# Optimization experiments

Measured on AMD Instinct MI355X. Metric: run time of the kernel, lower is better.

## Reference

```python
import jax, jax.numpy as jnp
import numpy as np

N = 262144          # total points
IN_DIM = 9
OUT_DIM = 256
FDIM = 128
MAX_PT = 64
B, GX, GY, GZ = 4, 64, 64, 16
EPS = 1e-5


def _linear_params(key, fin, fout):
    k1, k2 = jax.random.split(key)
    bound = 1.0 / np.sqrt(fin)
    w = jax.random.uniform(k1, (fin, fout), minval=-bound, maxval=bound, dtype=jnp.float32)
    b = jax.random.uniform(k2, (fout,), minval=-bound, maxval=bound, dtype=jnp.float32)
    return w, b


def setup_inputs() -> dict:
    key = jax.random.key(0)
    ks = jax.random.split(key, 12)
    pt_fea = jax.random.normal(ks[0], (N, IN_DIM), dtype=jnp.float32)
    bidx = jax.random.randint(ks[1], (N, 1), 0, B, dtype=jnp.int32)
    gx = jax.random.randint(ks[2], (N, 1), 0, GX, dtype=jnp.int32)
    gy = jax.random.randint(ks[3], (N, 1), 0, GY, dtype=jnp.int32)
    gz = jax.random.randint(ks[4], (N, 1), 0, GZ, dtype=jnp.int32)
    pt_ind = jnp.concatenate([bidx, gx, gy, gz], axis=1)
    # emulate torch.randperm shuffle (fixed seed)
    perm = jax.random.permutation(ks[5], N)
    pt_fea = pt_fea[perm]
    pt_ind = pt_ind[perm]
    w1, b1 = _linear_params(ks[6], IN_DIM, 64)
    w2, b2 = _linear_params(ks[7], 64, 128)
    w3, b3 = _linear_params(ks[8], 128, 256)
    w4, b4 = _linear_params(ks[9], 256, OUT_DIM)
    wc, bc = _linear_params(ks[10], OUT_DIM, FDIM)
    return {
        'pt_fea': pt_fea, 'pt_ind': pt_ind,
        'bn0_g': jnp.ones(IN_DIM), 'bn0_b': jnp.zeros(IN_DIM),
        'w1': w1, 'b1': b1, 'bn1_g': jnp.ones(64), 'bn1_b': jnp.zeros(64),
        'w2': w2, 'b2': b2, 'bn2_g': jnp.ones(128), 'bn2_b': jnp.zeros(128),
        'w3': w3, 'b3': b3, 'bn3_g': jnp.ones(256), 'bn3_b': jnp.zeros(256),
        'w4': w4, 'b4': b4, 'wc': wc, 'bc': bc,
    }


def _masked_bn(x, g, b, mf):
    # BatchNorm1d in training mode, statistics over kept points only (biased var)
    w = mf[:, None]
    n = jnp.sum(mf)
    mean = jnp.sum(x * w, axis=0) / n
    var = jnp.sum(jnp.square(x - mean) * w, axis=0) / n
    return (x - mean) * jax.lax.rsqrt(var + EPS) * g + b


def _grouping(pt_ind):
    # encode (batch, x, y, z) rows into a single int key; lexicographic order preserved
    keys = ((pt_ind[:, 0] * GX + pt_ind[:, 1]) * GY + pt_ind[:, 2]) * GZ + pt_ind[:, 3]
    unq, unq_inv = jnp.unique(keys, return_inverse=True, size=N, fill_value=-1)
    cnt = jax.ops.segment_sum(jnp.ones(N, jnp.int32), unq_inv, num_segments=N)
    valid = cnt > 0
    # rank of each point within its voxel group (stable order -> matches grp_range_torch)
    order = jnp.argsort(unq_inv, stable=True)
    sorted_inv = unq_inv[order]
    firstpos = jax.ops.segment_min(jnp.arange(N, dtype=jnp.int32), sorted_inv,
                                   num_segments=N, indices_are_sorted=True)
    grp_sorted = jnp.arange(N, dtype=jnp.int32) - firstpos[sorted_inv]
    grp = jnp.zeros(N, jnp.int32).at[order].set(grp_sorted)
    mask = grp < MAX_PT
    # decode unique keys back to coordinates [N, 4] (padded rows -> -1)
    z = unq % GZ; t = unq // GZ
    y = t % GY; t = t // GY
    x = t % GX; bb = t // GX
    coords = jnp.stack([bb, x, y, z], axis=1).astype(jnp.int64)
    coords = jnp.where(valid[:, None], coords, -1)
    return unq_inv, valid, mask, coords


def reference(pt_fea, pt_ind, bn0_g, bn0_b, w1, b1, bn1_g, bn1_b, w2, b2,
              bn2_g, bn2_b, w3, b3, bn3_g, bn3_b, w4, b4, wc, bc):
    unq_inv, valid, mask, coords = _grouping(pt_ind)
    mf = mask.astype(pt_fea.dtype)
    h = _masked_bn(pt_fea, bn0_g, bn0_b, mf)
    h = jax.nn.relu(_masked_bn(h @ w1 + b1, bn1_g, bn1_b, mf))
    h = jax.nn.relu(_masked_bn(h @ w2 + b2, bn2_g, bn2_b, mf))
    h = jax.nn.relu(_masked_bn(h @ w3 + b3, bn3_g, bn3_b, mf))
    h = h @ w4 + b4                                   # [N, OUT_DIM]
    feat = jnp.where(mask[:, None], h, -jnp.inf)      # drop points beyond MAX_PT per voxel
    pooled = jax.ops.segment_max(feat, unq_inv, num_segments=N)
    pooled = jnp.where(valid[:, None], pooled, 0.0)   # zero padded voxel slots
    voxel_features = jax.nn.relu(pooled @ wc + bc)    # [N, FDIM], rows beyond n_unique padded
    return coords, voxel_features
```

## Files before the change

### kernel.cpp

```cpp
#include <hip/hip_runtime.h>
#include <hip/hip_bf16.h>
#include <math.h>

#define N_PTS 262144
#define SBLOCKS 1024

typedef short short8 __attribute__((ext_vector_type(8)));
typedef float f32x4 __attribute__((ext_vector_type(4)));

__device__ __forceinline__ unsigned short f2bf(float f) {
    unsigned u = __float_as_uint(f);
    u = u + 0x7fff + ((u >> 16) & 1);
    return (unsigned short)(u >> 16);
}

__global__ void k_keys(const int* __restrict__ pt_ind, int* __restrict__ key, int* __restrict__ cnt) {
    int i = blockIdx.x * 256 + threadIdx.x;
    int b = pt_ind[i * 4 + 0], x = pt_ind[i * 4 + 1], y = pt_ind[i * 4 + 2], z = pt_ind[i * 4 + 3];
    int k = ((b * 64 + x) * 64 + y) * 16 + z;
    key[i] = k;
    atomicAdd(&cnt[k], 1);
}

__global__ __launch_bounds__(1024) void k_scan1(const int* __restrict__ cnt, int* __restrict__ rank,
                                                int* __restrict__ startb, int2* __restrict__ bsums) {
    __shared__ int so[1024], sc[1024];
    int t = threadIdx.x;
    int g = blockIdx.x * 1024 + t;
    int c = cnt[g];
    int o = (c > 0) ? 1 : 0;
    so[t] = o; sc[t] = c;
    __syncthreads();
    for (int off = 1; off < 1024; off <<= 1) {
        int vo = (t >= off) ? so[t - off] : 0;
        int vc = (t >= off) ? sc[t - off] : 0;
        __syncthreads();
        if (t >= off) { so[t] += vo; sc[t] += vc; }
        __syncthreads();
    }
    rank[g] = so[t] - o;
    startb[g] = sc[t] - c;
    if (t == 1023) bsums[blockIdx.x] = make_int2(so[t], sc[t]);
}

__global__ void k_scan2(int2* __restrict__ bsums, int* __restrict__ devU) {
    __shared__ int so[256], sc[256];
    int t = threadIdx.x;
    int2 v = bsums[t];
    so[t] = v.x; sc[t] = v.y;
    __syncthreads();
    for (int off = 1; off < 256; off <<= 1) {
        int vo = (t >= off) ? so[t - off] : 0;
        int vc = (t >= off) ? sc[t - off] : 0;
        __syncthreads();
        if (t >= off) { so[t] += vo; sc[t] += vc; }
        __syncthreads();
    }
    bsums[t] = make_int2(so[t] - v.x, sc[t] - v.y);
    if (t == 255) *devU = so[255];
}

__global__ __launch_bounds__(1024) void k_scan3(int* __restrict__ rank, int* __restrict__ startb,
                                                const int2* __restrict__ bsums) {
    int g = blockIdx.x * 1024 + threadIdx.x;
    int2 o = bsums[blockIdx.x];
    rank[g] += o.x;
    startb[g] += o.y;
}

__global__ void k_scatter(const int* __restrict__ key, const int* __restrict__ startb,
                          int* __restrict__ cursor, int* __restrict__ bucket) {
    int i = blockIdx.x * 256 + threadIdx.x;
    int k = key[i];
    int pos = startb[k] + atomicAdd(&cursor[k], 1);
    bucket[pos] = i;
}

__global__ void k_grouprank(const int* __restrict__ bucket, const int* __restrict__ key,
                            const int* __restrict__ cnt, const int* __restrict__ startb,
                            int* __restrict__ maskb_s, int* __restrict__ maskb_o,
                            int* __restrict__ n_masked) {
    int pos = blockIdx.x * 256 + threadIdx.x;
    int i = bucket[pos];
    int k = key[i];
    int s = startb[k];
    int c = cnt[k];
    int g = 0;
    for (int j = 0; j < c; j++) {
        int p = bucket[s + j];
        g += (p < i) ? 1 : 0;
    }
    int m = (g < 64) ? 1 : 0;
    maskb_s[pos] = m;
    maskb_o[i] = m;
    unsigned long long bal = __ballot(m);
    if ((threadIdx.x & 63) == 0) atomicAdd(n_masked, (int)__popcll(bal));
}

__global__ void k_coords(const int* __restrict__ cnt, const int* __restrict__ rank,
                         const int* __restrict__ startb, const int* __restrict__ devU,
                         float* __restrict__ out, int* __restrict__ ustart, int* __restrict__ ucnt) {
    int k = blockIdx.x * 256 + threadIdx.x;
    int U = *devU;
    if (cnt[k] > 0) {
        int r = rank[k];
        int z = k & 15;
        int t = k >> 4;
        int y = t & 63; t >>= 6;
        int x = t & 63;
        int b = t >> 6;
        out[r * 4 + 0] = (float)b;
        out[r * 4 + 1] = (float)x;
        out[r * 4 + 2] = (float)y;
        out[r * 4 + 3] = (float)z;
        ustart[r] = startb[k];
        ucnt[r] = cnt[k];
    }
    if (k >= U) {
        out[k * 4 + 0] = -1.f;
        out[k * 4 + 1] = -1.f;
        out[k * 4 + 2] = -1.f;
        out[k * 4 + 3] = -1.f;
    }
}

template<int F, int FP>
__global__ __launch_bounds__(256) void k_stats(const float* __restrict__ buf, const int* __restrict__ maskb,
                                               float* __restrict__ psum, float* __restrict__ psq) {
    constexpr int RG = 256 / FP;
    int tid = threadIdx.x;
    int col = tid % FP;
    int rg = tid / FP;
    constexpr int RPB = N_PTS / SBLOCKS;
    int r0 = blockIdx.x * RPB;
    float s = 0.f, q = 0.f;
    for (int r = r0 + rg; r < r0 + RPB; r += RG) {
        float mf = (float)maskb[r];
        if (col < F) {
            float v = buf[(size_t)r * F + col];
            s += v * mf;
            q += v * v * mf;
        }
    }
    __shared__ float ls[256], lq[256];
    ls[tid] = s; lq[tid] = q;
    __syncthreads();
    for (int half = RG / 2; half > 0; half >>= 1) {
        if (rg < half) { ls[tid] += ls[tid + half * FP]; lq[tid] += lq[tid + half * FP]; }
        __syncthreads();
    }
    if (rg == 0 && col < F) {
        psum[blockIdx.x * F + col] = ls[tid];
        psq[blockIdx.x * F + col] = lq[tid];
    }
}

template<int F, int NB>
__global__ __launch_bounds__(256) void k_finalize(const float* __restrict__ psum, const float* __restrict__ psq,
                                                  const int* __restrict__ n_masked, const float* __restrict__ g,
                                                  const float* __restrict__ b, float* __restrict__ ss) {
    int j = blockIdx.x;
    int t = threadIdx.x;
    double s = 0.0, q = 0.0;
    for (int i = t; i < NB; i += 256) {
        s += (double)psum[(size_t)i * F + j];
        q += (double)psq[(size_t)i * F + j];
    }
    __shared__ double ds[256], dq[256];
    ds[t] = s; dq[t] = q;
    __syncthreads();
    for (int half = 128; half > 0; half >>= 1) {
        if (t < half) { ds[t] += ds[t + half]; dq[t] += dq[t + half]; }
        __syncthreads();
    }
    if (t == 0) {
        double n = (double)(*n_masked);
        double mean = ds[0] / n;
        double var = dq[0] / n - mean * mean;
        if (var < 0.0) var = 0.0;
        double scale = (double)g[j] / sqrt(var + 1e-5);
        ss[j * 2] = (float)scale;
        ss[j * 2 + 1] = (float)((double)b[j] - mean * scale);
    }
}

template<int K, int F>
__global__ void k_wprep(const float* __restrict__ W, const float* __restrict__ ss,
                        unsigned short* __restrict__ WH, unsigned short* __restrict__ WL,
                        float* __restrict__ c0a, float* __restrict__ c1a) {
    int idx = blockIdx.x * 256 + threadIdx.x;
    if (idx >= K * F) return;
    int k = idx / F, f = idx % F;
    float s = 1.f, t = 0.f;
    if (ss) { s = ss[k * 2]; t = ss[k * 2 + 1]; }
    float sg = (s >= 0.f) ? 1.f : -1.f;
    float as = fabsf(s);
    float c1, c0;
    if (as < 1e-30f) { c1 = 0.f; c0 = fmaxf(t, 0.f); as = 1.f; }
    else { c1 = sg; c0 = t / as; }
    if (f == 0) { c0a[k] = c0; c1a[k] = c1; }
    float wv = as * W[(size_t)k * F + f];
    unsigned u = __float_as_uint(wv);
    unsigned hk = u & 0xFFFF0000u;
    float lo = wv - __uint_as_float(hk);
    WH[(size_t)f * K + k] = (unsigned short)(hk >> 16);
    WL[(size_t)f * K + k] = f2bf(lo);
}

__global__ __launch_bounds__(256) void k_mm1(const float* __restrict__ Af, const int* __restrict__ bucket,
                                             const float* __restrict__ W, const float* __restrict__ bias,
                                             const float* __restrict__ ss, const int* __restrict__ maskb_s,
                                             float* __restrict__ out,
                                             float* __restrict__ psum, float* __restrict__ psq) {
    constexpr int K = 9, F = 64, TM = 4, TN = 4;
    constexpr int SLOTS = F / TN;
    constexpr int RG = 256 / SLOTS;
    constexpr int MT = TM * RG;
    constexpr int STRIDE = 12;
    __shared__ float As[MT * STRIDE];
    __shared__ float msk[64];
    __shared__ float rs[4][256], rq[4][256];

    int tid = threadIdx.x;
    int row0 = blockIdx.x * MT;

    if (tid < 64) msk[tid] = (float)maskb_s[row0 + tid];
    for (int idx = tid; idx < MT * K; idx += 256) {
        int r = idx / K;
        int kk = idx % K;
        int src = bucket[row0 + r];
        float v = Af[(size_t)src * K + kk];
        v = v * ss[kk * 2] + ss[kk * 2 + 1];
        As[r * STRIDE + kk] = v;
    }
    __syncthreads();

    int slot = tid % SLOTS;
    int rg = tid / SLOTS;

    float acc[TM][TN];
    #pragma unroll
    for (int m = 0; m < TM; m++)
        #pragma unroll
        for (int i = 0; i < TN; i++) acc[m][i] = 0.f;

    #pragma unroll 3
    for (int k = 0; k < K; k++) {
        float w[TN];
        #pragma unroll
        for (int i = 0; i < TN; i++) w[i] = W[k * F + slot + i * SLOTS];
        #pragma unroll
        for (int m = 0; m < TM; m++) {
            float a = As[(rg * TM + m) * STRIDE + k];
            #pragma unroll
            for (int i = 0; i < TN; i++) acc[m][i] = fmaf(a, w[i], acc[m][i]);
        }
    }

    float s4[4] = {0.f, 0.f, 0.f, 0.f}, q4[4] = {0.f, 0.f, 0.f, 0.f};
    #pragma unroll
    for (int m = 0; m < TM; m++) {
        int r = row0 + rg * TM + m;
        float mf = msk[rg * TM + m];
        #pragma unroll
        for (int i = 0; i < TN; i++) {
            int c = slot + i * SLOTS;
            float v = acc[m][i] + bias[c];
            out[(size_t)r * F + c] = v;
            float t = mf * v;
            s4[i] += t;
            q4[i] += t * v;
        }
    }
    #pragma unroll
    for (int i = 0; i < 4; i++) { rs[i][tid] = s4[i]; rq[i][tid] = q4[i]; }
    __syncthreads();
    for (int half = 8; half > 0; half >>= 1) {
        if (rg < half) {
            #pragma unroll
            for (int i = 0; i < 4; i++) {
                rs[i][tid] += rs[i][tid + half * 16];
                rq[i][tid] += rq[i][tid + half * 16];
            }
        }
        __syncthreads();
    }
    if (rg == 0) {
        #pragma unroll
        for (int i = 0; i < 4; i++) {
            psum[(size_t)blockIdx.x * F + slot + i * 16] = rs[i][tid];
            psq[(size_t)blockIdx.x * F + slot + i * 16] = rq[i][tid];
        }
    }
}

template<int K, int F, int MODE, bool AMAX, bool TBL, bool STATS>
__global__ __launch_bounds__(2 * F) void k_gemm(const float* __restrict__ A,
                                                const unsigned short* __restrict__ WH,
                                                const unsigned short* __restrict__ WL,
                                                const float* __restrict__ c0a, const float* __restrict__ c1a,
                                                const float* __restrict__ bias, const int* __restrict__ devU,
                                                const int* __restrict__ maskb, float* __restrict__ out,
                                                float* __restrict__ psum, float* __restrict__ psq) {
    constexpr int THREADS = 2 * F;
    constexpr int RPASS = THREADS / 4;
    constexpr int NPASS = 128 / RPASS;
    __shared__ unsigned AsH[128 * 32], AsL[128 * 32];
    __shared__ float msk[128];
    __shared__ float sps[F], spq[F];
    const int tid = threadIdx.x;
    const int row0 = blockIdx.x * 128;
    const int w = tid >> 6, lane = tid & 63;
    const int wm = w & 1, wn = w >> 1;
    const int lr = lane & 15, lg = lane >> 4;
    const int r0 = tid >> 2, q0 = tid & 3;

    int U = 0x7fffffff;
    if constexpr (MODE == 2) {
        U = *devU;
        if (row0 >= U) {
            for (int idx = tid; idx < 128 * F; idx += THREADS) {
                int rr = idx / F, cc = idx % F;
                out[(size_t)(row0 + rr) * F + cc] = fmaxf(bias[cc], 0.f);
            }
            return;
        }
    }

    if constexpr (STATS) { if (tid < 128) msk[tid] = (float)maskb[row0 + tid]; }

    f32x4 acc[4][4];
    #pragma unroll
    for (int m = 0; m < 4; m++)
        #pragma unroll
        for (int n = 0; n < 4; n++) acc[m][n] = (f32x4)(0.f);

    float4 ld[NPASS][4];
    #pragma unroll
    for (int un = 0; un < NPASS; ++un) {
        const float4* p4 = (const float4*)(A + (size_t)(row0 + r0 + un * RPASS) * K + q0 * 16);
        #pragma unroll
        for (int p = 0; p < 4; ++p) ld[un][p] = p4[p];
    }

    for (int kc = 0; kc < K; kc += 64) {
        float4 tc0[4], tc1[4];
        if constexpr (TBL) {
            #pragma unroll
            for (int p = 0; p < 4; ++p) {
                tc0[p] = *(const float4*)&c0a[kc + q0 * 16 + p * 4];
                tc1[p] = *(const float4*)&c1a[kc + q0 * 16 + p * 4];
            }
        }
        __syncthreads();
        #pragma unroll
        for (int un = 0; un < NPASS; ++un) {
            int r = r0 + un * RPASS;
            unsigned swz = (unsigned)((r & 7) << 2);
            bool valid = true;
            if constexpr (MODE == 2) valid = (row0 + r) < U;
            unsigned uh[8], ul[8];
            #pragma unroll
            for (int p = 0; p < 4; ++p) {
                float zz[4] = {ld[un][p].x, ld[un][p].y, ld[un][p].z, ld[un][p].w};
                #pragma unroll
                for (int e = 0; e < 4; ++e) {
                    float z = zz[e];
                    if constexpr (MODE == 2) z = valid ? z : 0.f;
                    if constexpr (TBL) z = fmaf(z, (&tc1[p].x)[e], (&tc0[p].x)[e]);
                    if constexpr (AMAX) z = fmaxf(z, 0.f);
                    zz[e] = z;
                }
                #pragma unroll
                for (int h = 0; h < 2; ++h) {
                    unsigned u0 = __float_as_uint(zz[h * 2]), u1 = __float_as_uint(zz[h * 2 + 1]);
                    unsigned hi = (u1 & 0xFFFF0000u) | (u0 >> 16);
                    float l0 = zz[h * 2]     - __uint_as_float(u0 & 0xFFFF0000u);
                    float l1 = zz[h * 2 + 1] - __uint_as_float(u1 & 0xFFFF0000u);
                    unsigned lo = ((unsigned)f2bf(l1) << 16) | (unsigned)f2bf(l0);
                    uh[p * 2 + h] = hi;
                    ul[p * 2 + h] = lo;
                }
            }
            unsigned b0 = r * 32 + ((q0 * 8 + 0) ^ swz);
            unsigned b1 = r * 32 + ((q0 * 8 + 4) ^ swz);
            *(uint4*)&AsH[b0] = make_uint4(uh[0], uh[1], uh[2], uh[3]);
            *(uint4*)&AsH[b1] = make_uint4(uh[4], uh[5], uh[6], uh[7]);
            *(uint4*)&AsL[b0] = make_uint4(ul[0], ul[1], ul[2], ul[3]);
            *(uint4*)&AsL[b1] = make_uint4(ul[4], ul[5], ul[6], ul[7]);
        }
        __syncthreads();
        if (kc + 64 < K) {
            #pragma unroll
            for (int un = 0; un < NPASS; ++un) {
                const float4* p4 = (const float4*)(A + (size_t)(row0 + r0 + un * RPASS) * K + kc + 64 + q0 * 16);
                #pragma unroll
                for (int p = 0; p < 4; ++p) ld[un][p] = p4[p];
            }
        }
        #pragma unroll
        for (int kb = 0; kb < 2; ++kb) {
            short8 bh[4], bl[4];
            #pragma unroll
            for (int n = 0; n < 4; n++) {
                int c = wn * 64 + n * 16 + lr;
                size_t off = (size_t)c * K + kc + kb * 32 + lg * 8;
                bh[n] = *(const short8*)(WH + off);
                bl[n] = *(const short8*)(WL + off);
            }
            #pragma unroll
            for (int m = 0; m < 4; m++) {
                int rr = wm * 64 + m * 16 + lr;
                unsigned base = rr * 32 + ((kb * 16 + lg * 4) ^ ((unsigned)(rr & 7) << 2));
                short8 ah = *(const short8*)&AsH[base];
                short8 al = *(const short8*)&AsL[base];
                #pragma unroll
                for (int n = 0; n < 4; n++) {
                    acc[m][n] = __builtin_amdgcn_mfma_f32_16x16x32_bf16(ah, bh[n], acc[m][n], 0, 0, 0);
                    acc[m][n] = __builtin_amdgcn_mfma_f32_16x16x32_bf16(ah, bl[n], acc[m][n], 0, 0, 0);
                    acc[m][n] = __builtin_amdgcn_mfma_f32_16x16x32_bf16(al, bh[n], acc[m][n], 0, 0, 0);
                }
            }
        }
    }

    float bn[4];
    #pragma unroll
    for (int n = 0; n < 4; n++) bn[n] = bias[wn * 64 + n * 16 + lr];

    float s4[4] = {0.f, 0.f, 0.f, 0.f}, q4[4] = {0.f, 0.f, 0.f, 0.f};
    #pragma unroll
    for (int m = 0; m < 4; m++) {
        float mf[4];
        if constexpr (STATS) {
            #pragma unroll
            for (int reg = 0; reg < 4; reg++) mf[reg] = msk[wm * 64 + m * 16 + lg * 4 + reg];
        }
        #pragma unroll
        for (int n = 0; n < 4; n++) {
            int col = wn * 64 + n * 16 + lr;
            #pragma unroll
            for (int reg = 0; reg < 4; reg++) {
                int row = row0 + wm * 64 + m * 16 + lg * 4 + reg;
                float v = acc[m][n][reg] + bn[n];
                if constexpr (MODE == 2) v = fmaxf(v, 0.f);
                out[(size_t)row * F + col] = v;
                if constexpr (STATS) { float t = mf[reg] * v; s4[n] += t; q4[n] += t * v; }
            }
        }
    }

    if constexpr (STATS) {
        #pragma unroll
        for (int n = 0; n < 4; n++) {
            s4[n] += __shfl_xor(s4[n], 16); s4[n] += __shfl_xor(s4[n], 32);
            q4[n] += __shfl_xor(q4[n], 16); q4[n] += __shfl_xor(q4[n], 32);
        }
        if (wm == 0 && lg == 0) {
            #pragma unroll
            for (int n = 0; n < 4; n++) {
                int col = wn * 64 + n * 16 + lr;
                sps[col] = s4[n]; spq[col] = q4[n];
            }
        }
        __syncthreads();
        if (wm == 1 && lg == 0) {
            #pragma unroll
            for (int n = 0; n < 4; n++) {
                int col = wn * 64 + n * 16 + lr;
                psum[(size_t)blockIdx.x * F + col] = sps[col] + s4[n];
                psq[(size_t)blockIdx.x * F + col] = spq[col] + q4[n];
            }
        }
    }
}

__global__ __launch_bounds__(256) void k_pool(const float* __restrict__ h4,
                                              const int* __restrict__ ustart, const int* __restrict__ ucnt,
                                              const int* __restrict__ maskb_s, const int* __restrict__ devU,
                                              float* __restrict__ pooled) {
    int u = blockIdx.x * 4 + (threadIdx.x >> 6);
    if (u >= *devU) return;
    int lane = threadIdx.x & 63;
    int s = ustart[u], c = ucnt[u];
    float4 v = make_float4(-3.4e38f, -3.4e38f, -3.4e38f, -3.4e38f);
    for (int j = 0; j < c; ++j) {
        int row = s + j;
        if (maskb_s[row]) {
            float4 x = *(const float4*)&h4[(size_t)row * 256 + lane * 4];
            v.x = fmaxf(v.x, x.x);
            v.y = fmaxf(v.y, x.y);
            v.z = fmaxf(v.z, x.z);
            v.w = fmaxf(v.w, x.w);
        }
    }
    *(float4*)&pooled[(size_t)u * 256 + lane * 4] = v;
}

extern "C" void kernel_launch(void* const* d_in, const int* in_sizes, int n_in,
                              void* d_out, int out_size, void* d_ws, size_t ws_size,
                              hipStream_t stream) {
    const float* pt_fea = (const float*)d_in[0];
    const int*   pt_ind = (const int*)d_in[1];
    const float* bn0_g = (const float*)d_in[2];
    const float* bn0_b = (const float*)d_in[3];
    const float* w1 = (const float*)d_in[4];
    const float* b1 = (const float*)d_in[5];
    const float* bn1_g = (const float*)d_in[6];
    const float* bn1_b = (const float*)d_in[7];
    const float* w2 = (const float*)d_in[8];
    const float* b2 = (const float*)d_in[9];
    const float* bn2_g = (const float*)d_in[10];
    const float* bn2_b = (const float*)d_in[11];
    const float* w3 = (const float*)d_in[12];
    const float* b3 = (const float*)d_in[13];
    const float* bn3_g = (const float*)d_in[14];
    const float* bn3_b = (const float*)d_in[15];
    const float* w4 = (const float*)d_in[16];
    const float* b4 = (const float*)d_in[17];
    const float* wc = (const float*)d_in[18];
    const float* bc = (const float*)d_in[19];

    float* outF = (float*)d_out;
    float* coords_out = outF;
    float* feat_out = outF + (size_t)4 * N_PTS;

    char* wp = (char*)d_ws;
    auto alloc = [&](size_t bytes) {
        char* p = wp;
        wp += (bytes + 255) & ~(size_t)255;
        return p;
    };
    float* bufA = (float*)alloc((size_t)N_PTS * 256 * 4);
    float* bufB = (float*)alloc((size_t)N_PTS * 256 * 4);
    int* key     = (int*)alloc((size_t)N_PTS * 4);
    int* cnt     = (int*)alloc((size_t)N_PTS * 4);
    int* rank    = (int*)alloc((size_t)N_PTS * 4);
    int* startb  = (int*)alloc((size_t)N_PTS * 4);
    int* cursor  = (int*)alloc((size_t)N_PTS * 4);
    int* bucket  = (int*)alloc((size_t)N_PTS * 4);
    int* maskb_s = (int*)alloc((size_t)N_PTS * 4);
    int* maskb_o = (int*)alloc((size_t)N_PTS * 4);
    int* ustart  = (int*)alloc((size_t)N_PTS * 4);
    int* ucnt    = (int*)alloc((size_t)N_PTS * 4);
    int2* bsums  = (int2*)alloc(256 * sizeof(int2));
    int* devU    = (int*)alloc(256);
    int* n_masked= (int*)alloc(256);
    float* psum  = (float*)alloc((size_t)2048 * 256 * 4);
    float* psq   = (float*)alloc((size_t)2048 * 256 * 4);
    float* ss0   = (float*)alloc(2048);
    float* ss1   = (float*)alloc(2048);
    float* ss2   = (float*)alloc(2048);
    float* ss3   = (float*)alloc(2048);
    unsigned short* W2H = (unsigned short*)alloc(64 * 128 * 2);
    unsigned short* W2L = (unsigned short*)alloc(64 * 128 * 2);
    unsigned short* W3H = (unsigned short*)alloc(128 * 256 * 2);
    unsigned short* W3L = (unsigned short*)alloc(128 * 256 * 2);
    unsigned short* W4H = (unsigned short*)alloc(256 * 256 * 2);
    unsigned short* W4L = (unsigned short*)alloc(256 * 256 * 2);
    unsigned short* WCH = (unsigned short*)alloc(256 * 128 * 2);
    unsigned short* WCL = (unsigned short*)alloc(256 * 128 * 2);
    float* c02 = (float*)alloc(64 * 4);   float* c12 = (float*)alloc(64 * 4);
    float* c03 = (float*)alloc(128 * 4);  float* c13 = (float*)alloc(128 * 4);
    float* c04 = (float*)alloc(256 * 4);  float* c14 = (float*)alloc(256 * 4);
    float* c0c = (float*)alloc(256 * 4);  float* c1c = (float*)alloc(256 * 4);

    hipMemsetAsync(cnt, 0, (size_t)N_PTS * 4, stream);
    hipMemsetAsync(cursor, 0, (size_t)N_PTS * 4, stream);
    hipMemsetAsync(n_masked, 0, 4, stream);

    k_wprep<256, 128><<<(256 * 128 + 255) / 256, 256, 0, stream>>>(wc, nullptr, WCH, WCL, c0c, c1c);

    k_keys<<<N_PTS / 256, 256, 0, stream>>>(pt_ind, key, cnt);
    k_scan1<<<N_PTS / 1024, 1024, 0, stream>>>(cnt, rank, startb, bsums);
    k_scan2<<<1, 256, 0, stream>>>(bsums, devU);
    k_scan3<<<N_PTS / 1024, 1024, 0, stream>>>(rank, startb, bsums);
    k_scatter<<<N_PTS / 256, 256, 0, stream>>>(key, startb, cursor, bucket);
    k_grouprank<<<N_PTS / 256, 256, 0, stream>>>(bucket, key, cnt, startb, maskb_s, maskb_o, n_masked);
    k_coords<<<N_PTS / 256, 256, 0, stream>>>(cnt, rank, startb, devU, coords_out, ustart, ucnt);

    k_stats<9, 16><<<SBLOCKS, 256, 0, stream>>>(pt_fea, maskb_o, psum, psq);
    k_finalize<9, SBLOCKS><<<9, 256, 0, stream>>>(psum, psq, n_masked, bn0_g, bn0_b, ss0);

    k_mm1<<<N_PTS / 64, 256, 0, stream>>>(pt_fea, bucket, w1, b1, ss0, maskb_s, bufA, psum, psq);
    k_finalize<64, N_PTS / 64><<<64, 256, 0, stream>>>(psum, psq, n_masked, bn1_g, bn1_b, ss1);
    k_wprep<64, 128><<<(64 * 128 + 255) / 256, 256, 0, stream>>>(w2, ss1, W2H, W2L, c02, c12);

    k_gemm<64, 128, 0, true, true, true><<<N_PTS / 128, 256, 0, stream>>>(
        bufA, W2H, W2L, c02, c12, b2, nullptr, maskb_s, bufB, psum, psq);
    k_finalize<128, N_PTS / 128><<<128, 256, 0, stream>>>(psum, psq, n_masked, bn2_g, bn2_b, ss2);
    k_wprep<128, 256><<<(128 * 256 + 255) / 256, 256, 0, stream>>>(w3, ss2, W3H, W3L, c03, c13);

    k_gemm<128, 256, 0, true, true, true><<<N_PTS / 128, 512, 0, stream>>>(
        bufB, W3H, W3L, c03, c13, b3, nullptr, maskb_s, bufA, psum, psq);
    k_finalize<256, N_PTS / 128><<<256, 256, 0, stream>>>(psum, psq, n_masked, bn3_g, bn3_b, ss3);
    k_wprep<256, 256><<<(256 * 256 + 255) / 256, 256, 0, stream>>>(w4, ss3, W4H, W4L, c04, c14);

    k_gemm<256, 256, 0, true, true, false><<<N_PTS / 128, 512, 0, stream>>>(
        bufA, W4H, W4L, c04, c14, b4, nullptr, nullptr, bufB, nullptr, nullptr);

    k_pool<<<N_PTS / 4, 256, 0, stream>>>(bufB, ustart, ucnt, maskb_s, devU, bufA);

    k_gemm<256, 128, 2, false, false, false><<<N_PTS / 128, 256, 0, stream>>>(
        bufA, WCH, WCL, nullptr, nullptr, bc, devU, nullptr, feat_out, nullptr, nullptr);
}
```

Before: 925.9 us.

## Double-buffer A tiles and software-pipeline B fragment loads in split-bf16 GEMM

Restructures the GEMM kernel to always use 512 threads, with each wave covering F/4 columns. A tiles are double-buffered in shared memory, and the next tile is staged partway through the current MFMA batch. B fragments are prefetched one batch ahead in two register sets, and MFMA sections raise wave priority with s_setprio. The aim is to hide global and LDS latency behind matrix math and cut barrier stalls, at the cost of double the shared memory and higher register pressure from the 4-wave occupancy hint.

```diff
diff --git a/kernel.cpp b/kernel.cpp
--- a/kernel.cpp
+++ b/kernel.cpp
@@ -295,19 +295,21 @@
 }
 
 template<int K, int F, int MODE, bool AMAX, bool TBL, bool STATS>
-__global__ __launch_bounds__(2 * F) void k_gemm(const float* __restrict__ A,
-                                                const unsigned short* __restrict__ WH,
-                                                const unsigned short* __restrict__ WL,
-                                                const float* __restrict__ c0a, const float* __restrict__ c1a,
-                                                const float* __restrict__ bias, const int* __restrict__ devU,
-                                                const int* __restrict__ maskb, float* __restrict__ out,
-                                                float* __restrict__ psum, float* __restrict__ psq) {
-    constexpr int THREADS = 2 * F;
-    constexpr int RPASS = THREADS / 4;
-    constexpr int NPASS = 128 / RPASS;
-    __shared__ unsigned AsH[128 * 32], AsL[128 * 32];
-    __shared__ float msk[128];
-    __shared__ float sps[F], spq[F];
+__global__ __launch_bounds__(512, 4) void k_gemm(const float* __restrict__ A,
+                                                 const unsigned short* __restrict__ WH,
+                                                 const unsigned short* __restrict__ WL,
+                                                 const float* __restrict__ c0a, const float* __restrict__ c1a,
+                                                 const float* __restrict__ bias, const int* __restrict__ devU,
+                                                 const int* __restrict__ maskb, float* __restrict__ out,
+                                                 float* __restrict__ psum, float* __restrict__ psq) {
+    constexpr int NN = F / 64;
+    constexpr int NB2 = NN / 2;
+    constexpr int NBATCH = 2 * NB2;
+    constexpr int NKC = K / 64;
+    constexpr int FQ = F / 4;
+    __shared__ unsigned AsH[2 * 4096], AsL[2 * 4096];
+    __shared__ float msk[STATS ? 128 : 1];
+    __shared__ float sps[STATS ? F : 1], spq[STATS ? F : 1];
     const int tid = threadIdx.x;
     const int row0 = blockIdx.x * 128;
     const int w = tid >> 6, lane = tid & 63;
@@ -319,116 +321,123 @@
     if constexpr (MODE == 2) {
         U = *devU;
         if (row0 >= U) {
-            for (int idx = tid; idx < 128 * F; idx += THREADS) {
+            for (int idx = tid; idx < 128 * F; idx += 512) {
                 int rr = idx / F, cc = idx % F;
                 out[(size_t)(row0 + rr) * F + cc] = fmaxf(bias[cc], 0.f);
             }
             return;
         }
     }
-
     if constexpr (STATS) { if (tid < 128) msk[tid] = (float)maskb[row0 + tid]; }
 
-    f32x4 acc[4][4];
+    f32x4 acc[4][NN];
     #pragma unroll
     for (int m = 0; m < 4; m++)
         #pragma unroll
-        for (int n = 0; n < 4; n++) acc[m][n] = (f32x4)(0.f);
-
-    float4 ld[NPASS][4];
-    #pragma unroll
-    for (int un = 0; un < NPASS; ++un) {
-        const float4* p4 = (const float4*)(A + (size_t)(row0 + r0 + un * RPASS) * K + q0 * 16);
-        #pragma unroll
-        for (int p = 0; p < 4; ++p) ld[un][p] = p4[p];
-    }
-
-    for (int kc = 0; kc < K; kc += 64) {
-        float4 tc0[4], tc1[4];
-        if constexpr (TBL) {
-            #pragma unroll
-            for (int p = 0; p < 4; ++p) {
-                tc0[p] = *(const float4*)&c0a[kc + q0 * 16 + p * 4];
-                tc1[p] = *(const float4*)&c1a[kc + q0 * 16 + p * 4];
-            }
-        }
-        __syncthreads();
-        #pragma unroll
-        for (int un = 0; un < NPASS; ++un) {
-            int r = r0 + un * RPASS;
-            unsigned swz = (unsigned)((r & 7) << 2);
-            bool valid = true;
-            if constexpr (MODE == 2) valid = (row0 + r) < U;
-            unsigned uh[8], ul[8];
-            #pragma unroll
-            for (int p = 0; p < 4; ++p) {
-                float zz[4] = {ld[un][p].x, ld[un][p].y, ld[un][p].z, ld[un][p].w};
-                #pragma unroll
-                for (int e = 0; e < 4; ++e) {
-                    float z = zz[e];
-                    if constexpr (MODE == 2) z = valid ? z : 0.f;
-                    if constexpr (TBL) z = fmaf(z, (&tc1[p].x)[e], (&tc0[p].x)[e]);
-                    if constexpr (AMAX) z = fmaxf(z, 0.f);
-                    zz[e] = z;
-                }
-                #pragma unroll
-                for (int h = 0; h < 2; ++h) {
-                    unsigned u0 = __float_as_uint(zz[h * 2]), u1 = __float_as_uint(zz[h * 2 + 1]);
-                    unsigned hi = (u1 & 0xFFFF0000u) | (u0 >> 16);
-                    float l0 = zz[h * 2]     - __uint_as_float(u0 & 0xFFFF0000u);
-                    float l1 = zz[h * 2 + 1] - __uint_as_float(u1 & 0xFFFF0000u);
-                    unsigned lo = ((unsigned)f2bf(l1) << 16) | (unsigned)f2bf(l0);
-                    uh[p * 2 + h] = hi;
-                    ul[p * 2 + h] = lo;
-                }
-            }
-            unsigned b0 = r * 32 + ((q0 * 8 + 0) ^ swz);
-            unsigned b1 = r * 32 + ((q0 * 8 + 4) ^ swz);
-            *(uint4*)&AsH[b0] = make_uint4(uh[0], uh[1], uh[2], uh[3]);
-            *(uint4*)&AsH[b1] = make_uint4(uh[4], uh[5], uh[6], uh[7]);
-            *(uint4*)&AsL[b0] = make_uint4(ul[0], ul[1], ul[2], ul[3]);
-            *(uint4*)&AsL[b1] = make_uint4(ul[4], ul[5], ul[6], ul[7]);
-        }
-        __syncthreads();
-        if (kc + 64 < K) {
-            #pragma unroll
-            for (int un = 0; un < NPASS; ++un) {
-                const float4* p4 = (const float4*)(A + (size_t)(row0 + r0 + un * RPASS) * K + kc + 64 + q0 * 16);
-                #pragma unroll
-                for (int p = 0; p < 4; ++p) ld[un][p] = p4[p];
-            }
-        }
-        #pragma unroll
-        for (int kb = 0; kb < 2; ++kb) {
-            short8 bh[4], bl[4];
-            #pragma unroll
-            for (int n = 0; n < 4; n++) {
-                int c = wn * 64 + n * 16 + lr;
-                size_t off = (size_t)c * K + kc + kb * 32 + lg * 8;
-                bh[n] = *(const short8*)(WH + off);
-                bl[n] = *(const short8*)(WL + off);
-            }
+        for (int n = 0; n < NN; n++) acc[m][n] = (f32x4)(0.f);
+
+    float4 ld[4];
+    auto loadA = [&](int t) {
+        const float4* p4 = (const float4*)(A + (size_t)(row0 + r0) * K + t * 64 + q0 * 16);
+        #pragma unroll
+        for (int p = 0; p < 4; ++p) ld[p] = p4[p];
+    };
+    auto stageA = [&](int buf, int t) {
+        unsigned swz = (unsigned)((r0 & 7) << 2);
+        bool valid = true;
+        if constexpr (MODE == 2) valid = (row0 + r0) < U;
+        unsigned uh[8], ul[8];
+        #pragma unroll
+        for (int p = 0; p < 4; ++p) {
+            float4 tc0, tc1;
+            if constexpr (TBL) {
+                tc0 = *(const float4*)&c0a[t * 64 + q0 * 16 + p * 4];
+                tc1 = *(const float4*)&c1a[t * 64 + q0 * 16 + p * 4];
+            }
+            float zz[4] = {ld[p].x, ld[p].y, ld[p].z, ld[p].w};
+            #pragma unroll
+            for (int e = 0; e < 4; ++e) {
+                float z = zz[e];
+                if constexpr (MODE == 2) z = valid ? z : 0.f;
+                if constexpr (TBL) z = fmaf(z, (&tc1.x)[e], (&tc0.x)[e]);
+                if constexpr (AMAX) z = fmaxf(z, 0.f);
+                zz[e] = z;
+            }
+            #pragma unroll
+            for (int h = 0; h < 2; ++h) {
+                unsigned u0 = __float_as_uint(zz[h * 2]), u1 = __float_as_uint(zz[h * 2 + 1]);
+                unsigned hi = (u1 & 0xFFFF0000u) | (u0 >> 16);
+                float l0 = zz[h * 2]     - __uint_as_float(u0 & 0xFFFF0000u);
+                float l1 = zz[h * 2 + 1] - __uint_as_float(u1 & 0xFFFF0000u);
+                unsigned lo = ((unsigned)f2bf(l1) << 16) | (unsigned)f2bf(l0);
+                uh[p * 2 + h] = hi;
+                ul[p * 2 + h] = lo;
+            }
+        }
+        unsigned b0 = buf * 4096 + r0 * 32 + ((q0 * 8 + 0) ^ swz);
+        unsigned b1 = buf * 4096 + r0 * 32 + ((q0 * 8 + 4) ^ swz);
+        *(uint4*)&AsH[b0] = make_uint4(uh[0], uh[1], uh[2], uh[3]);
+        *(uint4*)&AsH[b1] = make_uint4(uh[4], uh[5], uh[6], uh[7]);
+        *(uint4*)&AsL[b0] = make_uint4(ul[0], ul[1], ul[2], ul[3]);
+        *(uint4*)&AsL[b1] = make_uint4(ul[4], ul[5], ul[6], ul[7]);
+    };
+
+    short8 bh[2][2], bl[2][2];
+    auto loadB = [&](int t, int b, int set) {
+        int kb = b / NB2, p = b % NB2;
+        #pragma unroll
+        for (int j = 0; j < 2; ++j) {
+            int col = wn * FQ + (p * 2 + j) * 16 + lr;
+            size_t off = (size_t)col * K + t * 64 + kb * 32 + lg * 8;
+            bh[set][j] = *(const short8*)(WH + off);
+            bl[set][j] = *(const short8*)(WL + off);
+        }
+    };
+
+    loadA(0);
+    loadB(0, 0, 0);
+    stageA(0, 0);
+    if (NKC > 1) loadA(1);
+
+    for (int t = 0; t < NKC; ++t) {
+        int cur = t & 1;
+        __syncthreads();
+        #pragma unroll
+        for (int b = 0; b < NBATCH; ++b) {
+            const int kb = b / NB2, p = b % NB2;
+            const int s = b & 1;
+            if (b + 1 < NBATCH) loadB(t, b + 1, s ^ 1);
+            else if (t + 1 < NKC) loadB(t + 1, 0, s ^ 1);
+            if (b == NB2 && t + 1 < NKC) {
+                stageA(cur ^ 1, t + 1);
+                if (t + 2 < NKC) loadA(t + 2);
+            }
+            __builtin_amdgcn_s_setprio(1);
             #pragma unroll
             for (int m = 0; m < 4; m++) {
                 int rr = wm * 64 + m * 16 + lr;
-                unsigned base = rr * 32 + ((kb * 16 + lg * 4) ^ ((unsigned)(rr & 7) << 2));
+                unsigned base = cur * 4096 + rr * 32 + ((kb * 16 + lg * 4) ^ ((unsigned)(rr & 7) << 2));
                 short8 ah = *(const short8*)&AsH[base];
                 short8 al = *(const short8*)&AsL[base];
                 #pragma unroll
-                for (int n = 0; n < 4; n++) {
-                    acc[m][n] = __builtin_amdgcn_mfma_f32_16x16x32_bf16(ah, bh[n], acc[m][n], 0, 0, 0);
-                    acc[m][n] = __builtin_amdgcn_mfma_f32_16x16x32_bf16(ah, bl[n], acc[m][n], 0, 0, 0);
-                    acc[m][n] = __builtin_amdgcn_mfma_f32_16x16x32_bf16(al, bh[n], acc[m][n], 0, 0, 0);
+                for (int j = 0; j < 2; j++) {
+                    int n = p * 2 + j;
+                    acc[m][n] = __builtin_amdgcn_mfma_f32_16x16x32_bf16(ah, bh[s][j], acc[m][n], 0, 0, 0);
+                    acc[m][n] = __builtin_amdgcn_mfma_f32_16x16x32_bf16(ah, bl[s][j], acc[m][n], 0, 0, 0);
+                    acc[m][n] = __builtin_amdgcn_mfma_f32_16x16x32_bf16(al, bh[s][j], acc[m][n], 0, 0, 0);
                 }
             }
-        }
-    }
-
-    float bn[4];
+            __builtin_amdgcn_s_setprio(0);
+        }
+    }
+
+    float bn[NN];
     #pragma unroll
-    for (int n = 0; n < 4; n++) bn[n] = bias[wn * 64 + n * 16 + lr];
-
-    float s4[4] = {0.f, 0.f, 0.f, 0.f}, q4[4] = {0.f, 0.f, 0.f, 0.f};
+    for (int n = 0; n < NN; n++) bn[n] = bias[wn * FQ + n * 16 + lr];
+
+    float s4[NN], q4[NN];
+    #pragma unroll
+    for (int n = 0; n < NN; n++) { s4[n] = 0.f; q4[n] = 0.f; }
     #pragma unroll
     for (int m = 0; m < 4; m++) {
         float mf[4];
@@ -437,37 +446,37 @@
             for (int reg = 0; reg < 4; reg++) mf[reg] = msk[wm * 64 + m * 16 + lg * 4 + reg];
         }
         #pragma unroll
-        for (int n = 0; n < 4; n++) {
-            int col = wn * 64 + n * 16 + lr;
+        for (int n = 0; n < NN; n++) {
+            int col = wn * FQ + n * 16 + lr;
             #pragma unroll
             for (int reg = 0; reg < 4; reg++) {
                 int row = row0 + wm * 64 + m * 16 + lg * 4 + reg;
                 float v = acc[m][n][reg] + bn[n];
                 if constexpr (MODE == 2) v = fmaxf(v, 0.f);
                 out[(size_t)row * F + col] = v;
-                if constexpr (STATS) { float t = mf[reg] * v; s4[n] += t; q4[n] += t * v; }
+                if constexpr (STATS) { float tt = mf[reg] * v; s4[n] += tt; q4[n] += tt * v; }
             }
         }
     }
 
     if constexpr (STATS) {
         #pragma unroll
-        for (int n = 0; n < 4; n++) {
+        for (int n = 0; n < NN; n++) {
             s4[n] += __shfl_xor(s4[n], 16); s4[n] += __shfl_xor(s4[n], 32);
             q4[n] += __shfl_xor(q4[n], 16); q4[n] += __shfl_xor(q4[n], 32);
         }
         if (wm == 0 && lg == 0) {
             #pragma unroll
-            for (int n = 0; n < 4; n++) {
-                int col = wn * 64 + n * 16 + lr;
+            for (int n = 0; n < NN; n++) {
+                int col = wn * FQ + n * 16 + lr;
                 sps[col] = s4[n]; spq[col] = q4[n];
             }
         }
         __syncthreads();
         if (wm == 1 && lg == 0) {
             #pragma unroll
-            for (int n = 0; n < 4; n++) {
-                int col = wn * 64 + n * 16 + lr;
+            for (int n = 0; n < NN; n++) {
+                int col = wn * FQ + n * 16 + lr;
                 psum[(size_t)blockIdx.x * F + col] = sps[col] + s4[n];
                 psq[(size_t)blockIdx.x * F + col] = spq[col] + q4[n];
             }
@@ -586,7 +595,7 @@
     k_finalize<64, N_PTS / 64><<<64, 256, 0, stream>>>(psum, psq, n_masked, bn1_g, bn1_b, ss1);
     k_wprep<64, 128><<<(64 * 128 + 255) / 256, 256, 0, stream>>>(w2, ss1, W2H, W2L, c02, c12);
 
-    k_gemm<64, 128, 0, true, true, true><<<N_PTS / 128, 256, 0, stream>>>(
+    k_gemm<64, 128, 0, true, true, true><<<N_PTS / 128, 512, 0, stream>>>(
         bufA, W2H, W2L, c02, c12, b2, nullptr, maskb_s, bufB, psum, psq);
     k_finalize<128, N_PTS / 128><<<128, 256, 0, stream>>>(psum, psq, n_masked, bn2_g, bn2_b, ss2);
     k_wprep<128, 256><<<(128 * 256 + 255) / 256, 256, 0, stream>>>(w3, ss2, W3H, W3L, c03, c13);
@@ -601,6 +610,6 @@
 
     k_pool<<<N_PTS / 4, 256, 0, stream>>>(bufB, ustart, ucnt, maskb_s, devU, bufA);
 
-    k_gemm<256, 128, 2, false, false, false><<<N_PTS / 128, 256, 0, stream>>>(
+    k_gemm<256, 128, 2, false, false, false><<<N_PTS / 128, 512, 0, stream>>>(
         bufA, WCH, WCL, nullptr, nullptr, bc, devU, nullptr, feat_out, nullptr, nullptr);
 }
```

Result: slower. 1.160 ms (+25.3%).
